# Performance work log

Hardware: AMD Instinct MI355X
Metric: run time of the kernel (lower is better)

## Reference

```python
import jax, jax.numpy as jnp
import numpy as np

MODES = 32
INPUT_MODES = 24
LAMBDA = 0.1
T_TOTAL = 1.0
EVAL_PTS = 200  # hardcoded in Circuit.forward


def _unitary_from_parameters(n, params):
    # Reconstruct a unitary from n**2-1 real SU(N)-generator coefficients:
    # Hermitian traceless H, then U = expm(iH) via eigh (differentiable).
    m = n * (n - 1) // 2
    re = params[:m]
    im = params[m:2 * m]
    d = params[2 * m:2 * m + n - 1]
    iu = jnp.triu_indices(n, 1)
    H = jnp.zeros((n, n), jnp.complex64).at[iu].set(re + 1j * im)
    H = H + H.conj().T
    diag = jnp.concatenate([d, -jnp.sum(d, keepdims=True)]).astype(jnp.complex64)
    H = H + jnp.diag(diag)
    w, V = jnp.linalg.eigh(H)  # H Hermitian
    return (V * jnp.exp(1j * w)[None, :]) @ V.conj().T


def setup_inputs() -> dict:
    key = jax.random.key(0)
    k1, k2, k3, k4, k5, k6 = jax.random.split(key, 6)
    B = 2048
    return {
        "A0_real": jax.random.normal(k1, (B, INPUT_MODES), jnp.float32),
        "A0_imag": jax.random.normal(k2, (B, INPUT_MODES), jnp.float32),
        "omega": jax.random.normal(k3, (MODES,), jnp.float32),
        "kappa": jax.random.uniform(k4, (MODES,), jnp.float32),
        "nonlinearity": jax.random.uniform(k5, (1,), jnp.float32),
        "params": (jax.random.uniform(k6, (MODES * MODES - 1,), jnp.float32) - 0.5) * (2.0 * np.pi),
    }


def reference(A0_real, A0_imag, omega, kappa, nonlinearity, params):
    c64 = jnp.complex64
    B = A0_real.shape[0]
    A0 = (A0_real + 1j * A0_imag).astype(c64)
    # pad: first input_modes from A0, rest ones (per forward)
    A_init = jnp.ones((B, MODES), c64).at[:, :INPUT_MODES].set(A0)

    U = _unitary_from_parameters(MODES, params)
    I = jnp.eye(MODES, dtype=c64)
    UtU = U.T @ U  # plain (non-conjugate) transpose, matching torch U.T
    mix = UtU @ jnp.linalg.inv(I * (1.0 + LAMBDA) - UtU)
    kappa2 = kappa.astype(c64) ** 2            # ode passes kappa**2
    sk = jnp.sqrt(kappa2)                      # diag_embed(kappa**0.5)
    T2 = -(sk[:, None] * (0.5 * I + mix)) * sk[None, :]  # constant in time
    nl2 = (nonlinearity[0].astype(c64)) ** 2   # ode passes nonlinearity**2
    om = omega.astype(c64)

    def f(A):  # time_evolution_operator, with diag matmuls fused elementwise
        freq = 1j * (om[None, :] + nl2 * (jnp.abs(A) ** 2))  # [B, modes]
        return freq * A + A @ T2.T  # correct_norm assumed identity passthrough

    dt = T_TOTAL / (EVAL_PTS - 1)

    def step(A, _):  # classic RK4 (fixed-step stand-in for dopri5)
        k1 = f(A)
        k2 = f(A + 0.5 * dt * k1)
        k3 = f(A + 0.5 * dt * k2)
        k4 = f(A + dt * k3)
        A = A + (dt / 6.0) * (k1 + 2.0 * k2 + 2.0 * k3 + k4)
        return A, A

    _, traj = jax.lax.scan(step, A_init, None, length=EVAL_PTS - 1)
    return jnp.concatenate([A_init[None], traj], axis=0)  # [200, B, modes] complex64
```

## Files before the change

### kernel.cpp

```cpp
#include <hip/hip_runtime.h>
#include <math.h>

#define NMODES 32
#define NPAIR 496
#define TAYLOR_N 12

__device__ float2 g_T2[NMODES * NMODES];

__device__ __forceinline__ float2 cmul(float2 a, float2 b) {
    return make_float2(a.x * b.x - a.y * b.y, a.x * b.y + a.y * b.x);
}

__global__ __launch_bounds__(1024) void setup_kernel(const float* __restrict__ params,
                                                     const float* __restrict__ kappa) {
    __shared__ float2 X[NMODES][NMODES];
    __shared__ float2 R[NMODES][NMODES];
    __shared__ float2 W[NMODES][NMODES];
    __shared__ float2 Aug[NMODES][2 * NMODES];
    __shared__ int sh_s;
    __shared__ float sh_scale;
    __shared__ int sh_piv;
    __shared__ float2 sh_pivrec;

    const int tid = threadIdx.x;
    const int i = tid >> 5;
    const int j = tid & 31;

    float2 h;
    if (i == j) {
        float d;
        if (i < 31) {
            d = params[2 * NPAIR + i];
        } else {
            d = 0.0f;
            for (int r = 0; r < 31; ++r) d -= params[2 * NPAIR + r];
        }
        h = make_float2(d, 0.0f);
    } else {
        int a = (i < j) ? i : j;
        int b = (i < j) ? j : i;
        int idx = 31 * a - (a * (a - 1)) / 2 + (b - a - 1);
        float re = params[idx];
        float im = params[NPAIR + idx];
        h = (i < j) ? make_float2(re, im) : make_float2(re, -im);
    }
    X[i][j] = h;
    __syncthreads();

    if (tid < 32) {
        float s = 0.0f;
        for (int c = 0; c < NMODES; ++c) {
            float2 v = X[tid][c];
            s += sqrtf(v.x * v.x + v.y * v.y);
        }
        for (int off = 16; off > 0; off >>= 1)
            s = fmaxf(s, __shfl_down(s, off));
        if (tid == 0) {
            int sc_n = 0;
            float sc = 1.0f;
            while (s > 0.25f && sc_n < 40) { s *= 0.5f; sc *= 0.5f; ++sc_n; }
            sh_s = sc_n;
            sh_scale = sc;
        }
    }
    __syncthreads();

    {
        float sc = sh_scale;
        float2 v = X[i][j];
        X[i][j] = make_float2(-v.y * sc, v.x * sc);
    }
    __syncthreads();

    R[i][j] = make_float2((i == j) ? 1.0f : 0.0f, 0.0f);
    __syncthreads();
    for (int k = TAYLOR_N; k >= 1; --k) {
        float2 acc = make_float2(0.0f, 0.0f);
        for (int kk = 0; kk < NMODES; ++kk) {
            float2 a = X[i][kk];
            float2 b = R[kk][j];
            acc.x = fmaf(a.x, b.x, fmaf(-a.y, b.y, acc.x));
            acc.y = fmaf(a.x, b.y, fmaf(a.y, b.x, acc.y));
        }
        __syncthreads();
        float invk = 1.0f / (float)k;
        R[i][j] = make_float2(((i == j) ? 1.0f : 0.0f) + acc.x * invk, acc.y * invk);
        __syncthreads();
    }

    {
        int s = sh_s;
        for (int q = 0; q < s; ++q) {
            float2 acc = make_float2(0.0f, 0.0f);
            for (int kk = 0; kk < NMODES; ++kk) {
                float2 a = R[i][kk];
                float2 b = R[kk][j];
                acc.x = fmaf(a.x, b.x, fmaf(-a.y, b.y, acc.x));
                acc.y = fmaf(a.x, b.y, fmaf(a.y, b.x, acc.y));
            }
            __syncthreads();
            R[i][j] = acc;
            __syncthreads();
        }
    }

    {
        float2 acc = make_float2(0.0f, 0.0f);
        for (int kk = 0; kk < NMODES; ++kk) {
            float2 a = R[kk][i];
            float2 b = R[kk][j];
            acc.x = fmaf(a.x, b.x, fmaf(-a.y, b.y, acc.x));
            acc.y = fmaf(a.x, b.y, fmaf(a.y, b.x, acc.y));
        }
        W[i][j] = acc;
    }
    __syncthreads();

    {
        float2 w = W[i][j];
        Aug[i][j] = make_float2(((i == j) ? 1.1f : 0.0f) - w.x, -w.y);
        Aug[i][j + NMODES] = w;
    }
    __syncthreads();

    for (int p = 0; p < NMODES; ++p) {
        if (tid < 32) {
            float2 v = Aug[tid][p];
            float mag = (tid >= p) ? (v.x * v.x + v.y * v.y) : -1.0f;
            int idx = tid;
            for (int off = 16; off > 0; off >>= 1) {
                float omg = __shfl_down(mag, off);
                int oi = __shfl_down(idx, off);
                if (omg > mag) { mag = omg; idx = oi; }
            }
            if (tid == 0) sh_piv = idx;
        }
        __syncthreads();
        int piv = sh_piv;
        if (piv != p && i == p) {
            float2 a0 = Aug[p][j], b0 = Aug[piv][j];
            float2 a1 = Aug[p][j + NMODES], b1 = Aug[piv][j + NMODES];
            Aug[p][j] = b0; Aug[piv][j] = a0;
            Aug[p][j + NMODES] = b1; Aug[piv][j + NMODES] = a1;
        }
        __syncthreads();
        if (tid == 0) {
            float2 d = Aug[p][p];
            float den = d.x * d.x + d.y * d.y;
            sh_pivrec = make_float2(d.x / den, -d.y / den);
        }
        __syncthreads();
        if (i == p) {
            float2 pr = sh_pivrec;
            Aug[p][j] = cmul(Aug[p][j], pr);
            Aug[p][j + NMODES] = cmul(Aug[p][j + NMODES], pr);
        }
        __syncthreads();
        float2 f = Aug[i][p];
        __syncthreads();
        if (i != p) {
            float2 rp0 = Aug[p][j];
            float2 rp1 = Aug[p][j + NMODES];
            float2 v0 = Aug[i][j];
            float2 v1 = Aug[i][j + NMODES];
            v0.x -= f.x * rp0.x - f.y * rp0.y;
            v0.y -= f.x * rp0.y + f.y * rp0.x;
            v1.x -= f.x * rp1.x - f.y * rp1.y;
            v1.y -= f.x * rp1.y + f.y * rp1.x;
            Aug[i][j] = v0;
            Aug[i][j + NMODES] = v1;
        }
        __syncthreads();
    }

    {
        float2 mix = Aug[i][j + NMODES];
        float kk2 = fabsf(kappa[i]) * fabsf(kappa[j]);
        float re = -kk2 * (((i == j) ? 0.5f : 0.0f) + mix.x);
        float im = -kk2 * mix.y;
        g_T2[i * NMODES + j] = make_float2(re, im);
    }
}


template<int CTRL>
__device__ __forceinline__ float2 dppshuf(float2 v) {
    return make_float2(
        __int_as_float(__builtin_amdgcn_mov_dpp(__float_as_int(v.x), CTRL, 0xF, 0xF, true)),
        __int_as_float(__builtin_amdgcn_mov_dpp(__float_as_int(v.y), CTRL, 0xF, 0xF, true)));
}

#define QP_X1 0xB1
#define QP_X2 0x4E
#define QP_X3 0x1B
#define HM_X7 0x141
#define RM_XF 0x140

__device__ __forceinline__ void cfma(float2& acc, float2 c, float2 w) {
    acc.x = fmaf(c.x, w.x, fmaf(-c.y, w.y, acc.x));
    acc.y = fmaf(c.x, w.y, fmaf(c.y, w.x, acc.y));
}

__device__ __forceinline__ float bperm(int idx, float v) {
    return __int_as_float(__builtin_amdgcn_ds_bpermute(idx, __float_as_int(v)));
}

__device__ __forceinline__ float2 feval_dpp(const float2* __restrict__ t2,
                                            float2 z, float om, float nl2,
                                            int bp0, int bp1) {
    float2 w1 = dppshuf<QP_X1>(z);
    float2 w2 = dppshuf<QP_X2>(z);
    float2 w3 = dppshuf<QP_X3>(z);
    float2 w7 = dppshuf<HM_X7>(z);
    float2 wF = dppshuf<RM_XF>(z);
    float2 w4 = dppshuf<QP_X3>(w7);
    float2 w5 = dppshuf<QP_X2>(w7);
    float2 w6 = dppshuf<QP_X1>(w7);
    float2 w8 = dppshuf<HM_X7>(wF);
    float2 wC = dppshuf<QP_X3>(wF);
    float2 wD = dppshuf<QP_X2>(wF);
    float2 wE = dppshuf<QP_X1>(wF);
    float2 w9 = dppshuf<QP_X1>(w8);
    float2 wA = dppshuf<QP_X2>(w8);
    float2 wB = dppshuf<QP_X3>(w8);

    float2 a0 = make_float2(0.0f, 0.0f), a1 = make_float2(0.0f, 0.0f);
    float2 a2 = make_float2(0.0f, 0.0f), a3 = make_float2(0.0f, 0.0f);
    cfma(a0, t2[0],  z);
    cfma(a1, t2[1],  w1);
    cfma(a2, t2[2],  w2);
    cfma(a3, t2[3],  w3);
    cfma(a0, t2[4],  w4);
    cfma(a1, t2[5],  w5);
    cfma(a2, t2[6],  w6);
    cfma(a3, t2[7],  w7);
    cfma(a0, t2[8],  w8);
    cfma(a1, t2[9],  w9);
    cfma(a2, t2[10], wA);
    cfma(a3, t2[11], wB);
    cfma(a0, t2[12], wC);
    cfma(a1, t2[13], wD);
    cfma(a2, t2[14], wE);
    cfma(a3, t2[15], wF);

    float px = (a0.x + a1.x) + (a2.x + a3.x);
    float py = (a0.y + a1.y) + (a2.y + a3.y);
    float kx = bperm(bp0, px) + bperm(bp1, px);
    float ky = bperm(bp0, py) + bperm(bp1, py);

    float wf = fmaf(nl2, fmaf(z.x, z.x, z.y * z.y), om);
    return make_float2(kx - wf * z.y, ky + wf * z.x);
}

__device__ void ode_dpp(int b, int lane,
                        const float* __restrict__ A0r,
                        const float* __restrict__ A0i,
                        const float* __restrict__ omega,
                        const float* __restrict__ nln,
                        float* __restrict__ out, long long out_size) {
    const int r = lane >> 4;
    const int p = lane & 15;
    const int ho = r & 1;
    const int hr = (r == 1 || r == 2) ? 1 : 0;
    const int mstar = 16 * hr + p;
    const int bp0 = 4 * mstar;
    const int bp1 = bp0 + 128;

    float2 t2[16];
    {
        const int row_g = 16 * ho + p;
#pragma unroll
        for (int s = 0; s < 16; ++s)
            t2[s] = g_T2[row_g * 32 + 16 * hr + (p ^ s)];
    }

    const float om = omega[mstar];
    const float nl = nln[0];
    const float nl2 = nl * nl;
    const float dt = 1.0f / 199.0f;
    const float hdt = 0.5f * dt;
    const float sdt = dt / 6.0f;

    __shared__ float2 ainit[32];
    if (lane < 32) {
        float2 v;
        if (lane < 24) v = make_float2(A0r[b * 24 + lane], A0i[b * 24 + lane]);
        else           v = make_float2(1.0f, 0.0f);
        ainit[lane] = v;
    }
    __syncthreads();
    float2 a = ainit[mstar];

    long long o = (long long)b * 32 + lane;
    if (lane < 32 && o < out_size) out[o] = a.x;

    for (int t = 1; t < 200; ++t) {
        float2 k1 = feval_dpp(t2, a, om, nl2, bp0, bp1);
        float2 z = make_float2(fmaf(hdt, k1.x, a.x), fmaf(hdt, k1.y, a.y));
        float2 k2 = feval_dpp(t2, z, om, nl2, bp0, bp1);
        z = make_float2(fmaf(hdt, k2.x, a.x), fmaf(hdt, k2.y, a.y));
        float2 k3 = feval_dpp(t2, z, om, nl2, bp0, bp1);
        z = make_float2(fmaf(dt, k3.x, a.x), fmaf(dt, k3.y, a.y));
        float2 k4 = feval_dpp(t2, z, om, nl2, bp0, bp1);

        a.x = fmaf(sdt, fmaf(2.0f, k2.x + k3.x, k1.x + k4.x), a.x);
        a.y = fmaf(sdt, fmaf(2.0f, k2.y + k3.y, k1.y + k4.y), a.y);

        o += 65536;
        if (lane < 32 && o < out_size) out[o] = a.x;
    }
}

__device__ __forceinline__ float2 f_eval_lds(const float4* __restrict__ xq,
                                             float2 ym,
                                             const float2* __restrict__ t2h,
                                             float om, float nl2) {
    float2 acc0 = make_float2(0.0f, 0.0f);
    float2 acc1 = make_float2(0.0f, 0.0f);
#pragma unroll
    for (int j = 0; j < 8; ++j) {
        float4 v = xq[j];
        float2 ta = t2h[2 * j];
        float2 tb = t2h[2 * j + 1];
        acc0.x = fmaf(ta.x, v.x, acc0.x);
        acc0.x = fmaf(-ta.y, v.y, acc0.x);
        acc0.y = fmaf(ta.x, v.y, acc0.y);
        acc0.y = fmaf(ta.y, v.x, acc0.y);
        acc1.x = fmaf(tb.x, v.z, acc1.x);
        acc1.x = fmaf(-tb.y, v.w, acc1.x);
        acc1.y = fmaf(tb.x, v.w, acc1.y);
        acc1.y = fmaf(tb.y, v.z, acc1.y);
    }
    float2 acc = make_float2(acc0.x + acc1.x, acc0.y + acc1.y);
    acc.x += __shfl_xor(acc.x, 1);
    acc.y += __shfl_xor(acc.y, 1);
    float w = fmaf(nl2, fmaf(ym.x, ym.x, ym.y * ym.y), om);
    return make_float2(acc.x - w * ym.y, acc.y + w * ym.x);
}

__device__ void ode_lds(int b, int lane,
                        const float* __restrict__ A0r,
                        const float* __restrict__ A0i,
                        const float* __restrict__ omega,
                        const float* __restrict__ nln,
                        float* __restrict__ out, long long out_size) {
    const int m = lane >> 1;
    const int h = lane & 1;

    float2 t2h[16];
#pragma unroll
    for (int j = 0; j < 16; ++j) t2h[j] = g_T2[m * NMODES + h * 16 + j];

    const float om = omega[m];
    const float nl = nln[0];
    const float nl2 = nl * nl;
    const float dt = 1.0f / 199.0f;
    const float hdt = 0.5f * dt;
    const float sdt = dt / 6.0f;

    float2 a;
    if (m < 24) a = make_float2(A0r[b * 24 + m], A0i[b * 24 + m]);
    else        a = make_float2(1.0f, 0.0f);

    __shared__ __align__(16) float2 xbuf[36];
    const int swi = m + ((m >= 16) ? 2 : 0);
    const float4* xq = reinterpret_cast<const float4*>(xbuf) + 9 * h;

    if (h == 0) {
        long long o0 = (long long)b * 32 + m;
        if (o0 < out_size) out[o0] = a.x;
        xbuf[swi] = a;
    }
    __syncthreads();

    long long o = (long long)b * 32 + m;
    for (int t = 1; t < 200; ++t) {
        float2 k1 = f_eval_lds(xq, a, t2h, om, nl2);
        float2 y2 = make_float2(fmaf(hdt, k1.x, a.x), fmaf(hdt, k1.y, a.y));
        if (h == 0) xbuf[swi] = y2;
        __syncthreads();

        float2 k2 = f_eval_lds(xq, y2, t2h, om, nl2);
        float2 y3 = make_float2(fmaf(hdt, k2.x, a.x), fmaf(hdt, k2.y, a.y));
        if (h == 0) xbuf[swi] = y3;
        __syncthreads();

        float2 k3 = f_eval_lds(xq, y3, t2h, om, nl2);
        float2 y4 = make_float2(fmaf(dt, k3.x, a.x), fmaf(dt, k3.y, a.y));
        if (h == 0) xbuf[swi] = y4;
        __syncthreads();

        float2 k4 = f_eval_lds(xq, y4, t2h, om, nl2);

        a.x = fmaf(sdt, k1.x + 2.0f * k2.x + 2.0f * k3.x + k4.x, a.x);
        a.y = fmaf(sdt, k1.y + 2.0f * k2.y + 2.0f * k3.y + k4.y, a.y);

        o += 65536;
        if (h == 0) {
            xbuf[swi] = a;
            if (o < out_size) out[o] = a.x;
        }
        __syncthreads();
    }
}

__global__ __launch_bounds__(64) void ode_kernel(const float* __restrict__ A0r,
                                                 const float* __restrict__ A0i,
                                                 const float* __restrict__ omega,
                                                 const float* __restrict__ nln,
                                                 float* __restrict__ out,
                                                 long long out_size) {
    const int lane = threadIdx.x;
    const int b = blockIdx.x;
    if ((b & 1) == 0) {
        ode_dpp(b, lane, A0r, A0i, omega, nln, out, out_size);
    } else {
        ode_lds(b, lane, A0r, A0i, omega, nln, out, out_size);
    }
}

extern "C" void kernel_launch(void* const* d_in, const int* in_sizes, int n_in,
                              void* d_out, int out_size, void* d_ws, size_t ws_size,
                              hipStream_t stream) {
    const float* A0r = (const float*)d_in[0];
    const float* A0i = (const float*)d_in[1];
    const float* omega = (const float*)d_in[2];
    const float* kappa = (const float*)d_in[3];
    const float* nln = (const float*)d_in[4];
    const float* params = (const float*)d_in[5];

    setup_kernel<<<1, 1024, 0, stream>>>(params, kappa);
    ode_kernel<<<2048, 64, 0, stream>>>(A0r, A0i, omega, nln,
                                        (float*)d_out, (long long)out_size);
}
```

Measured before the change: 393.8 us.

## Pair DPP and LDS waves in one block and use wave barriers

Launches 1024 blocks of 128 threads, with one wave running the DPP-based ODE path and the other the LDS-based path, instead of 2048 single-wave blocks that alternate paths. Block-wide __syncthreads calls in the LDS path become wave-level barriers, since each wave only shares data within itself, and the DPP path's initial-state broadcast uses bperm in place of shared memory plus a barrier. The aim is to cut barrier overhead and ensure both path types are co-scheduled on each CU. It relies on wave barriers being enough to order the LDS writes and reads within a wave.

```diff
diff --git a/kernel.cpp b/kernel.cpp
--- a/kernel.cpp
+++ b/kernel.cpp
@@ -281,15 +281,10 @@
     const float hdt = 0.5f * dt;
     const float sdt = dt / 6.0f;
 
-    __shared__ float2 ainit[32];
-    if (lane < 32) {
-        float2 v;
-        if (lane < 24) v = make_float2(A0r[b * 24 + lane], A0i[b * 24 + lane]);
-        else           v = make_float2(1.0f, 0.0f);
-        ainit[lane] = v;
-    }
-    __syncthreads();
-    float2 a = ainit[mstar];
+    float ldr, ldi;
+    if (lane < 24) { ldr = A0r[b * 24 + lane]; ldi = A0i[b * 24 + lane]; }
+    else           { ldr = 1.0f;               ldi = 0.0f; }
+    float2 a = make_float2(bperm(4 * mstar, ldr), bperm(4 * mstar, ldi));
 
     long long o = (long long)b * 32 + lane;
     if (lane < 32 && o < out_size) out[o] = a.x;
@@ -310,6 +305,8 @@
         if (lane < 32 && o < out_size) out[o] = a.x;
     }
 }
+
+__device__ __forceinline__ void wb() { __builtin_amdgcn_wave_barrier(); }
 
 __device__ __forceinline__ float2 f_eval_lds(const float4* __restrict__ xq,
                                              float2 ym,
@@ -371,24 +368,24 @@
         if (o0 < out_size) out[o0] = a.x;
         xbuf[swi] = a;
     }
-    __syncthreads();
+    wb();
 
     long long o = (long long)b * 32 + m;
     for (int t = 1; t < 200; ++t) {
         float2 k1 = f_eval_lds(xq, a, t2h, om, nl2);
         float2 y2 = make_float2(fmaf(hdt, k1.x, a.x), fmaf(hdt, k1.y, a.y));
         if (h == 0) xbuf[swi] = y2;
-        __syncthreads();
+        wb();
 
         float2 k2 = f_eval_lds(xq, y2, t2h, om, nl2);
         float2 y3 = make_float2(fmaf(hdt, k2.x, a.x), fmaf(hdt, k2.y, a.y));
         if (h == 0) xbuf[swi] = y3;
-        __syncthreads();
+        wb();
 
         float2 k3 = f_eval_lds(xq, y3, t2h, om, nl2);
         float2 y4 = make_float2(fmaf(dt, k3.x, a.x), fmaf(dt, k3.y, a.y));
         if (h == 0) xbuf[swi] = y4;
-        __syncthreads();
+        wb();
 
         float2 k4 = f_eval_lds(xq, y4, t2h, om, nl2);
 
@@ -400,22 +397,23 @@
             xbuf[swi] = a;
             if (o < out_size) out[o] = a.x;
         }
-        __syncthreads();
-    }
-}
-
-__global__ __launch_bounds__(64) void ode_kernel(const float* __restrict__ A0r,
-                                                 const float* __restrict__ A0i,
-                                                 const float* __restrict__ omega,
-                                                 const float* __restrict__ nln,
-                                                 float* __restrict__ out,
-                                                 long long out_size) {
-    const int lane = threadIdx.x;
+        wb();
+    }
+}
+
+__global__ __launch_bounds__(128) void ode_kernel(const float* __restrict__ A0r,
+                                                  const float* __restrict__ A0i,
+                                                  const float* __restrict__ omega,
+                                                  const float* __restrict__ nln,
+                                                  float* __restrict__ out,
+                                                  long long out_size) {
+    const int tid = threadIdx.x;
+    const int lane = tid & 63;
     const int b = blockIdx.x;
-    if ((b & 1) == 0) {
+    if (tid < 64) {
         ode_dpp(b, lane, A0r, A0i, omega, nln, out, out_size);
     } else {
-        ode_lds(b, lane, A0r, A0i, omega, nln, out, out_size);
+        ode_lds(b + 1024, lane, A0r, A0i, omega, nln, out, out_size);
     }
 }
 
@@ -430,6 +428,6 @@
     const float* params = (const float*)d_in[5];
 
     setup_kernel<<<1, 1024, 0, stream>>>(params, kappa);
-    ode_kernel<<<2048, 64, 0, stream>>>(A0r, A0i, omega, nln,
-                                        (float*)d_out, (long long)out_size);
-}
+    ode_kernel<<<1024, 128, 0, stream>>>(A0r, A0i, omega, nln,
+                                         (float*)d_out, (long long)out_size);
+}
```

Measured after the change: 407.1 us. +3.4%, slower.
